# Performance work log

Hardware: AMD Instinct MI355X
Metric: run time of the kernel (lower is better)

Reference implementation:

```python
import jax, jax.numpy as jnp
import numpy as np

B, T, D, H = 8, 4096, 512, 512


def log_g(x):
    # log of g(x) where g(x) = relu(x) + 0.5 for x >= 0, sigmoid(x) for x < 0
    return jnp.where(x >= 0, jnp.log(jax.nn.relu(x) + 0.5), -jax.nn.softplus(-x))


def setup_inputs() -> dict:
    key = jax.random.key(0)
    kx, kh0, kwz, kbz, kwh, kbh = jax.random.split(key, 6)
    s = 1.0 / np.sqrt(D)
    return {
        "x": jax.random.normal(kx, (B, T, D), dtype=jnp.float32),
        "h_0": jax.random.uniform(kh0, (B, H), dtype=jnp.float32),
        "Wz": jax.random.uniform(kwz, (H, D), dtype=jnp.float32, minval=-s, maxval=s),
        "bz": jax.random.uniform(kbz, (H,), dtype=jnp.float32, minval=-s, maxval=s),
        "Wh": jax.random.uniform(kwh, (H, D), dtype=jnp.float32, minval=-s, maxval=s),
        "bh": jax.random.uniform(kbh, (H,), dtype=jnp.float32, minval=-s, maxval=s),
    }


def parallel_scan_log(log_coeffs, log_values):
    # log_coeffs: (B, T, H), log_values: (B, T+1, H)
    a_star = jnp.cumsum(jnp.pad(log_coeffs, ((0, 0), (1, 0), (0, 0))), axis=1)  # (B, T+1, H)
    log_h = a_star + jax.lax.cumlogsumexp(log_values - a_star, axis=1)
    return jnp.exp(log_h)  # (B, T+1, H)


def reference(x, h_0, Wz, bz, Wh, bh):
    k = jnp.einsum('btd,hd->bth', x, Wz) + bz                # (B, T, H)
    log_z = -jax.nn.softplus(-k)                              # log sigmoid(k)
    log_coeffs = -jax.nn.softplus(k)                          # log (1 - sigmoid(k))
    log_h0 = log_g(h_0)[:, None, :]                           # (B, 1, H)
    log_tilde_h = log_g(jnp.einsum('btd,hd->bth', x, Wh) + bh)
    vals = jnp.concatenate([log_h0, log_z + log_tilde_h], axis=1)  # (B, T+1, H)
    h = parallel_scan_log(log_coeffs, vals)
    return h[:, -x.shape[1]:, :]                              # (B, T, H)
```

## Files before the change

### kernel.cpp

```cpp
#include <hip/hip_runtime.h>
#include <math.h>

#define Bq 8
#define Tq 4096
#define Dq 512
#define Hq 512
#define Mq (Bq * Tq)
#define NC 64
#define CL 64

typedef unsigned short ushort_t;
typedef unsigned int uint_t;
typedef __bf16 bf16x8 __attribute__((ext_vector_type(8)));
typedef float f32x4 __attribute__((ext_vector_type(4)));

__device__ __forceinline__ ushort_t f2bf(float f) {
    unsigned int u = __float_as_uint(f);
    unsigned int r = u + 0x7fffu + ((u >> 16) & 1u);
    return (ushort_t)(r >> 16);
}

__device__ __forceinline__ void gload16(const void* g, void* l) {
    __builtin_amdgcn_global_load_lds(
        (const __attribute__((address_space(1))) void*)g,
        (__attribute__((address_space(3))) void*)l, 16, 0, 0);
}

__device__ __forceinline__ void gates(uint_t w, float& c, float& v) {
    float k  = __uint_as_float((w & 0xffffu) << 16);
    float th = __uint_as_float(w & 0xffff0000u);
    float ek = __expf(k);
    c = 1.0f / (1.0f + ek);
    float z = 1.0f - c;
    float g = (th >= 0.0f) ? (th + 0.5f) : (1.0f / (1.0f + __expf(-th)));
    v = z * g;
}

__global__ __launch_bounds__(256)
void convert_all(const float* __restrict__ x, const float* __restrict__ Wz,
                 const float* __restrict__ Wh, ushort_t* __restrict__ dst) {
    size_t i8 = ((size_t)blockIdx.x * 256 + threadIdx.x) * 8;
    const size_t XN = (size_t)Mq * Dq;
    const size_t WN = (size_t)Hq * Dq;
    const float* src; size_t off;
    if (i8 < XN)            { src = x;  off = i8; }
    else if (i8 < XN + WN)  { src = Wz; off = i8 - XN; }
    else                    { src = Wh; off = i8 - XN - WN; }
    float4 a = *reinterpret_cast<const float4*>(src + off);
    float4 b = *reinterpret_cast<const float4*>(src + off + 4);
    uint4 o;
    o.x = (uint_t)f2bf(a.x) | ((uint_t)f2bf(a.y) << 16);
    o.y = (uint_t)f2bf(a.z) | ((uint_t)f2bf(a.w) << 16);
    o.z = (uint_t)f2bf(b.x) | ((uint_t)f2bf(b.y) << 16);
    o.w = (uint_t)f2bf(b.z) | ((uint_t)f2bf(b.w) << 16);
    *reinterpret_cast<uint4*>(dst + i8) = o;
}

__global__ __launch_bounds__(256, 2)
void gemm_fused(const ushort_t* __restrict__ xb, const ushort_t* __restrict__ wb,
                const float* __restrict__ bz, const float* __restrict__ bh,
                uint_t* __restrict__ kvout, float2* __restrict__ chAW) {
    __shared__ __align__(16) ushort_t smem[3 * 128 * 64];
    ushort_t* As  = smem;
    ushort_t* Bzs = smem + 128 * 64;
    ushort_t* Bhs = smem + 2 * 128 * 64;

    const int tid  = threadIdx.x;
    const int lane = tid & 63;
    const int wave = tid >> 6;
    const int wm = (wave >> 1) * 64;
    const int wn = (wave & 1) * 64;
    const int mBase = blockIdx.x * 128;
    const int nBase = blockIdx.y * 128;
    const ushort_t* Wzb = wb;
    const ushort_t* Whb = wb + (size_t)Hq * Dq;

    f32x4 zero = {0.f, 0.f, 0.f, 0.f};
    f32x4 accz[4][4], acch[4][4];
#pragma unroll
    for (int i = 0; i < 4; ++i)
#pragma unroll
        for (int j = 0; j < 4; ++j) { accz[i][j] = zero; acch[i][j] = zero; }

    const int rowInW = lane >> 3;
    const int ccG = (lane & 7) ^ rowInW;
    const int swz = lane & 7;

    for (int k0 = 0; k0 < Dq; k0 += 64) {
#pragma unroll
        for (int j = 0; j < 4; ++j) {
            const int rseg = j * 4 + wave;
            const int row  = rseg * 8 + rowInW;
            const size_t gcol = (size_t)(k0 + ccG * 8);
            gload16(xb  + (size_t)(mBase + row) * Dq + gcol, &As [rseg * 512]);
            gload16(Wzb + (size_t)(nBase + row) * Dq + gcol, &Bzs[rseg * 512]);
            gload16(Whb + (size_t)(nBase + row) * Dq + gcol, &Bhs[rseg * 512]);
        }
        __syncthreads();

#pragma unroll
        for (int ks = 0; ks < 2; ++ks) {
            const int cc = ks * 4 + (lane >> 4);
            const int sc = cc ^ swz;
            bf16x8 af[4], bzf[4], bhf[4];
#pragma unroll
            for (int i = 0; i < 4; ++i) {
                int rowA = wm + i * 16 + (lane & 15);
                af[i] = *reinterpret_cast<const bf16x8*>(&As[rowA * 64 + sc * 8]);
            }
#pragma unroll
            for (int i = 0; i < 4; ++i) {
                int rowB = wn + i * 16 + (lane & 15);
                bzf[i] = *reinterpret_cast<const bf16x8*>(&Bzs[rowB * 64 + sc * 8]);
                bhf[i] = *reinterpret_cast<const bf16x8*>(&Bhs[rowB * 64 + sc * 8]);
            }
#pragma unroll
            for (int mi = 0; mi < 4; ++mi)
#pragma unroll
                for (int ni = 0; ni < 4; ++ni) {
                    accz[mi][ni] = __builtin_amdgcn_mfma_f32_16x16x32_bf16(
                        af[mi], bzf[ni], accz[mi][ni], 0, 0, 0);
                    acch[mi][ni] = __builtin_amdgcn_mfma_f32_16x16x32_bf16(
                        af[mi], bhf[ni], acch[mi][ni], 0, 0, 0);
                }
        }
        __syncthreads();
    }

    const int colL = lane & 15;
    const int quad = lane >> 4;
    float2* sb = reinterpret_cast<float2*>(smem) + wave * 1024;

#pragma unroll
    for (int ni = 0; ni < 4; ++ni) {
        int h = nBase + wn + ni * 16 + colL;
        float bzv = bz[h];
        float bhv = bh[h];
#pragma unroll
        for (int mi = 0; mi < 4; ++mi) {
            float A = 1.f, W = 0.f;
#pragma unroll
            for (int r = 0; r < 4; ++r) {
                int bt = mBase + wm + mi * 16 + quad * 4 + r;
                float kf  = accz[mi][ni][r] + bzv;
                float thf = acch[mi][ni][r] + bhv;
                uint_t word = (uint_t)f2bf(kf) | ((uint_t)f2bf(thf) << 16);
                kvout[(size_t)bt * Hq + h] = word;
                float c, v;
                gates(word, c, v);
                W = fmaf(c, W, v);
                A *= c;
            }
            sb[(mi * 4 + quad) * 64 + ni * 16 + colL] = make_float2(A, W);
        }
    }
    __syncthreads();
    {
        float A = 1.f, W = 0.f;
#pragma unroll
        for (int s = 0; s < 16; ++s) {
            float2 aw = sb[s * 64 + lane];
            W = fmaf(aw.x, W, aw.y);
            A *= aw.x;
        }
        int g = blockIdx.x * 2 + (wm >> 6);
        int h = nBase + wn + lane;
        chAW[(size_t)g * Hq + h] = make_float2(A, W);
    }
}

__global__ __launch_bounds__(256)
void scan_combine(const float* __restrict__ h0, const float2* __restrict__ chAW,
                  float* __restrict__ hstart) {
    int idx = blockIdx.x * 256 + threadIdx.x;
    int b = idx >> 9;
    int h = idx & (Hq - 1);
    float x0 = h0[idx];
    float r = (x0 >= 0.f) ? (x0 + 0.5f) : (1.f / (1.f + __expf(-x0)));
    const float2* p = chAW + (size_t)b * NC * Hq + h;
    for (int c0 = 0; c0 < NC; c0 += 16) {
        float2 aw[16];
#pragma unroll
        for (int j = 0; j < 16; ++j) aw[j] = p[(size_t)(c0 + j) * Hq];
#pragma unroll
        for (int j = 0; j < 16; ++j) {
            hstart[((size_t)b * NC + c0 + j) * Hq + h] = r;
            r = fmaf(aw[j].x, r, aw[j].y);
        }
    }
}

__global__ __launch_bounds__(256)
void scan_final(const uint_t* kv, const float* __restrict__ hstart, float* out) {
    const int b = blockIdx.x >> 6;
    const int chunk = blockIdx.x & 63;
    const int h2 = threadIdx.x;
    float2 hs = reinterpret_cast<const float2*>(hstart)[(size_t)blockIdx.x * (Hq / 2) + h2];
    float r0 = hs.x, r1 = hs.y;
    const uint2* kv2 = reinterpret_cast<const uint2*>(kv);
    float2* out2 = reinterpret_cast<float2*>(out);
    size_t base = ((size_t)b * Tq + (size_t)chunk * CL) * (Hq / 2) + h2;

    uint2 w[8];
#pragma unroll
    for (int j = 0; j < 8; ++j) w[j] = kv2[base + (size_t)j * (Hq / 2)];

    for (int bt = 0; bt < 8; ++bt) {
        uint2 wn[8];
        if (bt < 7) {
#pragma unroll
            for (int j = 0; j < 8; ++j)
                wn[j] = kv2[base + (size_t)((bt + 1) * 8 + j) * (Hq / 2)];
        }
#pragma unroll
        for (int j = 0; j < 8; ++j) {
            float c0, v0, c1, v1;
            gates(w[j].x, c0, v0);
            gates(w[j].y, c1, v1);
            r0 = fmaf(c0, r0, v0);
            r1 = fmaf(c1, r1, v1);
            out2[base + (size_t)(bt * 8 + j) * (Hq / 2)] = make_float2(r0, r1);
        }
#pragma unroll
        for (int j = 0; j < 8; ++j) w[j] = wn[j];
    }
}

extern "C" void kernel_launch(void* const* d_in, const int* in_sizes, int n_in,
                              void* d_out, int out_size, void* d_ws, size_t ws_size,
                              hipStream_t stream) {
    const float* x  = (const float*)d_in[0];
    const float* h0 = (const float*)d_in[1];
    const float* Wz = (const float*)d_in[2];
    const float* bz = (const float*)d_in[3];
    const float* Wh = (const float*)d_in[4];
    const float* bh = (const float*)d_in[5];
    float* out = (float*)d_out;

    char* ws = (char*)d_ws;
    ushort_t* xb = (ushort_t*)ws;
    ushort_t* wb = xb + (size_t)Mq * Dq;
    float2* chAW = (float2*)(wb + 2 * (size_t)Hq * Dq);
    float* hstart = (float*)((char*)chAW + (size_t)Bq * NC * Hq * sizeof(float2));
    uint_t* kv = (uint_t*)d_out;

    const int totalConv = (Mq * Dq + 2 * Hq * Dq) / (256 * 8);
    convert_all<<<dim3(totalConv), dim3(256), 0, stream>>>(x, Wz, Wh, xb);
    gemm_fused<<<dim3(Mq / 128, Hq / 128), dim3(256), 0, stream>>>(xb, wb, bz, bh, kv, chAW);
    scan_combine<<<dim3((Bq * Hq) / 256), dim3(256), 0, stream>>>(h0, chAW, hstart);
    scan_final<<<dim3(Bq * NC), dim3(256), 0, stream>>>(kv, hstart, out);
}
```

Before: 198.0 us.

## Fuse chunk-carry combine into final scan kernel, removing separate launch

Removes the scan_combine kernel and its hstart buffer. Each scan_final block now recomputes its own starting state by folding all preceding chunk (A,W) pairs sequentially from h0. Blocks are ordered so high-chunk blocks launch first, and each thread handles one hidden unit with 512 threads per block. This saves a launch and a global round-trip, but adds redundant serial prefix work (up to 63 dependent FMAs with loads) per block.

After: 197.3 us. Within noise of the previous version (-0.4%).

```diff
diff --git a/kernel.cpp b/kernel.cpp
--- a/kernel.cpp
+++ b/kernel.cpp
@@ -169,60 +169,53 @@
     }
 }
 
-__global__ __launch_bounds__(256)
-void scan_combine(const float* __restrict__ h0, const float2* __restrict__ chAW,
-                  float* __restrict__ hstart) {
-    int idx = blockIdx.x * 256 + threadIdx.x;
-    int b = idx >> 9;
-    int h = idx & (Hq - 1);
-    float x0 = h0[idx];
+__global__ __launch_bounds__(512)
+void scan_final(const uint_t* kv, const float* __restrict__ h0,
+                const float2* __restrict__ chAW, float* out) {
+    const int b = blockIdx.x & 7;
+    const int chunk = 63 - (blockIdx.x >> 3);
+    const int h = threadIdx.x;
+
+    float x0 = h0[(size_t)b * Hq + h];
     float r = (x0 >= 0.f) ? (x0 + 0.5f) : (1.f / (1.f + __expf(-x0)));
+
     const float2* p = chAW + (size_t)b * NC * Hq + h;
-    for (int c0 = 0; c0 < NC; c0 += 16) {
-        float2 aw[16];
-#pragma unroll
-        for (int j = 0; j < 16; ++j) aw[j] = p[(size_t)(c0 + j) * Hq];
-#pragma unroll
-        for (int j = 0; j < 16; ++j) {
-            hstart[((size_t)b * NC + c0 + j) * Hq + h] = r;
-            r = fmaf(aw[j].x, r, aw[j].y);
-        }
-    }
-}
-
-__global__ __launch_bounds__(256)
-void scan_final(const uint_t* kv, const float* __restrict__ hstart, float* out) {
-    const int b = blockIdx.x >> 6;
-    const int chunk = blockIdx.x & 63;
-    const int h2 = threadIdx.x;
-    float2 hs = reinterpret_cast<const float2*>(hstart)[(size_t)blockIdx.x * (Hq / 2) + h2];
-    float r0 = hs.x, r1 = hs.y;
-    const uint2* kv2 = reinterpret_cast<const uint2*>(kv);
-    float2* out2 = reinterpret_cast<float2*>(out);
-    size_t base = ((size_t)b * Tq + (size_t)chunk * CL) * (Hq / 2) + h2;
-
-    uint2 w[8];
-#pragma unroll
-    for (int j = 0; j < 8; ++j) w[j] = kv2[base + (size_t)j * (Hq / 2)];
-
-    for (int bt = 0; bt < 8; ++bt) {
-        uint2 wn[8];
-        if (bt < 7) {
-#pragma unroll
-            for (int j = 0; j < 8; ++j)
-                wn[j] = kv2[base + (size_t)((bt + 1) * 8 + j) * (Hq / 2)];
-        }
-#pragma unroll
-        for (int j = 0; j < 8; ++j) {
-            float c0, v0, c1, v1;
-            gates(w[j].x, c0, v0);
-            gates(w[j].y, c1, v1);
-            r0 = fmaf(c0, r0, v0);
-            r1 = fmaf(c1, r1, v1);
-            out2[base + (size_t)(bt * 8 + j) * (Hq / 2)] = make_float2(r0, r1);
-        }
-#pragma unroll
-        for (int j = 0; j < 8; ++j) w[j] = wn[j];
+    int j = 0;
+    for (; j + 8 <= chunk; j += 8) {
+        float2 aw[8];
+#pragma unroll
+        for (int q = 0; q < 8; ++q) aw[q] = p[(size_t)(j + q) * Hq];
+#pragma unroll
+        for (int q = 0; q < 8; ++q) r = fmaf(aw[q].x, r, aw[q].y);
+    }
+    for (; j < chunk; ++j) {
+        float2 aw = p[(size_t)j * Hq];
+        r = fmaf(aw.x, r, aw.y);
+    }
+
+    const size_t base = ((size_t)b * Tq + (size_t)chunk * CL) * Hq + h;
+    const uint_t* kvp = kv + base;
+    float* op = out + base;
+
+    uint_t w[16];
+#pragma unroll
+    for (int q = 0; q < 16; ++q) w[q] = kvp[(size_t)q * Hq];
+    for (int bt = 0; bt < 4; ++bt) {
+        uint_t wn[16];
+        if (bt < 3) {
+#pragma unroll
+            for (int q = 0; q < 16; ++q)
+                wn[q] = kvp[(size_t)((bt + 1) * 16 + q) * Hq];
+        }
+#pragma unroll
+        for (int q = 0; q < 16; ++q) {
+            float c, v;
+            gates(w[q], c, v);
+            r = fmaf(c, r, v);
+            op[(size_t)(bt * 16 + q) * Hq] = r;
+        }
+#pragma unroll
+        for (int q = 0; q < 16; ++q) w[q] = wn[q];
     }
 }
 
@@ -241,12 +234,10 @@
     ushort_t* xb = (ushort_t*)ws;
     ushort_t* wb = xb + (size_t)Mq * Dq;
     float2* chAW = (float2*)(wb + 2 * (size_t)Hq * Dq);
-    float* hstart = (float*)((char*)chAW + (size_t)Bq * NC * Hq * sizeof(float2));
     uint_t* kv = (uint_t*)d_out;
 
     const int totalConv = (Mq * Dq + 2 * Hq * Dq) / (256 * 8);
     convert_all<<<dim3(totalConv), dim3(256), 0, stream>>>(x, Wz, Wh, xb);
     gemm_fused<<<dim3(Mq / 128, Hq / 128), dim3(256), 0, stream>>>(xb, wb, bz, bh, kv, chAW);
-    scan_combine<<<dim3((Bq * Hq) / 256), dim3(256), 0, stream>>>(h0, chAW, hstart);
-    scan_final<<<dim3(Bq * NC), dim3(256), 0, stream>>>(kv, hstart, out);
-}
+    scan_final<<<dim3(Bq * NC), dim3(512), 0, stream>>>(kv, h0, chAW, out);
+}
```
